# Optimization experiments

Measured on AMD Instinct MI355X. Metric: run time of the kernel, lower is better.

The kernel has to match this reference:

```python
import jax, jax.numpy as jnp
import numpy as np
import math


def _sinusoidal_pe(seq_len, hidden_dim, dtype):
    pos = jnp.arange(seq_len, dtype=jnp.float32)[:, None]              # [S,1]
    div = jnp.exp(jnp.arange(0, hidden_dim, 2, dtype=jnp.float32) * (-math.log(10000.0) / hidden_dim))  # [H/2]
    ang = pos * div                                                    # [S,H/2]
    pe = jnp.stack([jnp.sin(ang), jnp.cos(ang)], axis=-1).reshape(seq_len, hidden_dim)  # interleave sin/cos
    return pe.astype(dtype)


def setup_inputs() -> dict:
    key = jax.random.key(0)
    ks = jax.random.split(key, 12)
    B, S, H = 4, 2048, 1024
    scale = 1.0 / math.sqrt(H)
    inp = {
        "x": jax.random.normal(ks[0], (B, S, H), dtype=jnp.float32),
        "mask": jax.random.randint(ks[1], (B, S, S), 0, 2, dtype=jnp.int32),
        "Wq": jax.random.normal(ks[2], (H, H), dtype=jnp.float32) * scale,
        "bq": jax.random.normal(ks[3], (H,), dtype=jnp.float32) * 0.02,
        "Wk": jax.random.normal(ks[4], (H, H), dtype=jnp.float32) * scale,
        "bk": jax.random.normal(ks[5], (H,), dtype=jnp.float32) * 0.02,
        "Wv": jax.random.normal(ks[6], (H, H), dtype=jnp.float32) * scale,
        "bv": jax.random.normal(ks[7], (H,), dtype=jnp.float32) * 0.02,
        "pos_bias": jax.random.normal(ks[8], (S, S), dtype=jnp.float32),
        "Wo": jax.random.normal(ks[9], (H, H), dtype=jnp.float32) * scale,
        "bo": jax.random.normal(ks[10], (H,), dtype=jnp.float32) * 0.02,
        "gamma": jnp.ones((H,), dtype=jnp.float32),
        "beta": jnp.zeros((H,), dtype=jnp.float32),
    }
    return inp


def reference(x, mask, Wq, bq, Wk, bk, Wv, bv, pos_bias, Wo, bo, gamma, beta):
    B, S, H = x.shape
    scale = math.sqrt(H)
    pe = _sinusoidal_pe(S, H, x.dtype)                  # [S,H]
    xp = x + pe[None, :, :]                             # [B,S,H]
    # torch Linear: y = x @ W.T + b
    q = jnp.einsum('bsh,oh->bso', xp, Wq) + bq
    k = jnp.einsum('bsh,oh->bso', xp, Wk) + bk
    v = jnp.einsum('bsh,oh->bso', xp, Wv) + bv
    scores = jnp.einsum('bqh,bkh->bqk', q, k) / scale   # [B,S,S]
    scores = scores + pos_bias[None, :S, :S]
    scores = jnp.where(mask == 0, jnp.asarray(-1e9, scores.dtype), scores)
    attn = jax.nn.softmax(scores, axis=-1)              # dropout = identity (eval mode)
    context = jnp.einsum('bqk,bkh->bqh', attn, v)
    out = jnp.einsum('bsh,oh->bso', context, Wo) + bo
    # LayerNorm(out + x)
    h = out + x
    mu = jnp.mean(h, axis=-1, keepdims=True)
    var = jnp.var(h, axis=-1, keepdims=True)
    normed = (h - mu) * jax.lax.rsqrt(var + 1e-5) * gamma + beta
    return normed, attn
```

## Files before the change

### kernel.cpp

```cpp
#include <hip/hip_runtime.h>
#include <hip/hip_bf16.h>
#include <math.h>

typedef __hip_bfloat16 bf16;
typedef __bf16 bf16x8 __attribute__((ext_vector_type(8)));
typedef float f32x4 __attribute__((ext_vector_type(4)));

static constexpr int  B_  = 4, S_ = 2048, H_ = 1024;
static constexpr long BSH = (long)B_ * S_ * H_;
static constexpr long SH  = (long)S_ * H_;
static constexpr long SS  = (long)S_ * S_;
static constexpr long HH  = (long)H_ * H_;

#define GLOAD_LDS16(gp, lp)                                                          \
  __builtin_amdgcn_global_load_lds((__attribute__((address_space(1))) void*)(gp),    \
                                   (__attribute__((address_space(3))) void*)(lp),    \
                                   16, 0, 0)

#define BARRIER() do { __builtin_amdgcn_s_barrier(); asm volatile("" ::: "memory"); } while (0)

template <int N> __device__ __forceinline__ void waitcnt_vm() {
  if constexpr (N == 0)      asm volatile("s_waitcnt vmcnt(0)" ::: "memory");
  else if constexpr (N == 3) asm volatile("s_waitcnt vmcnt(3)" ::: "memory");
  else if constexpr (N == 4) asm volatile("s_waitcnt vmcnt(4)" ::: "memory");
  else if constexpr (N == 6) asm volatile("s_waitcnt vmcnt(6)" ::: "memory");
  else if constexpr (N == 8) asm volatile("s_waitcnt vmcnt(8)" ::: "memory");
}

__device__ __forceinline__ float wave_reduce_sum(float v) {
#pragma unroll
  for (int o = 32; o; o >>= 1) v += __shfl_xor(v, o, 64);
  return v;
}
__device__ __forceinline__ float bf16r(float v) {
  return __bfloat162float(__float2bfloat16(v));
}

__global__ void prep_kernel(const float* __restrict__ Wq, const float* __restrict__ Wk,
                            const float* __restrict__ Wv, const float* __restrict__ Wo,
                            bf16* __restrict__ wdst,
                            const float* __restrict__ x, bf16* __restrict__ xpb) {
  const int bx  = blockIdx.x;
  const int tid = threadIdx.x;
  if (bx < 4096) {
    const int w = bx >> 10;
    const float* src = (w == 0) ? Wq : (w == 1) ? Wk : (w == 2) ? Wv : Wo;
    bf16* d = wdst + (long)w * HH;
    const int idx = ((bx & 1023) << 8) + tid;
    const float4 f = ((const float4*)src)[idx];
    d[idx * 4 + 0] = __float2bfloat16(f.x);
    d[idx * 4 + 1] = __float2bfloat16(f.y);
    d[idx * 4 + 2] = __float2bfloat16(f.z);
    d[idx * 4 + 3] = __float2bfloat16(f.w);
  } else {
    const long idx = (((long)(bx - 4096)) << 8) + tid;
    const int  i   = (int)(idx & (H_ / 2 - 1));
    const long bs  = idx >> 9;
    const int  s   = (int)(bs & (S_ - 1));
    const float div = __expf((float)(2 * i) * (-9.210340371976184f / (float)H_));
    const float ang = (float)s * div;
    const float2 xv = ((const float2*)x)[idx];
    xpb[idx * 2 + 0] = __float2bfloat16(xv.x + sinf(ang));
    xpb[idx * 2 + 1] = __float2bfloat16(xv.y + cosf(ang));
  }
}

template <int MODE, int BN>
__global__ __launch_bounds__(512, 2)
void gemm_nt(const bf16* __restrict__ A, long strideA,
             const bf16* __restrict__ Bm, long strideB,
             bf16* __restrict__ Cb, float* __restrict__ Cf, long sC,
             int M, int N, int K,
             const float* __restrict__ bias0,
             const float* __restrict__ bias1,
             const float* __restrict__ bias2,
             const float* __restrict__ pos_bias,
             const int* __restrict__ mask,
             const float* __restrict__ xres,
             const float* __restrict__ inv_sum) {
  constexpr int BM = 256, BK = 32;
  constexpr int FN    = BN / 64;
  constexpr int LPT_B = BN * BK * 2 / 8192;
  constexpr int LPT   = 2 + LPT_B;

  __shared__ bf16 sA[4][BM * BK];
  __shared__ bf16 sB[4][BN * BK];

  const int t    = threadIdx.x;
  const int lane = t & 63;
  const int wave = t >> 6;
  const int wm   = wave >> 2;
  const int wn   = wave & 3;
  const int z    = blockIdx.z;
  const int m0   = blockIdx.x * BM;
  const int n0   = blockIdx.y * BN;

  const bf16* Ab = A  + (long)z * strideA;
  const bf16* Bb = Bm + (long)z * strideB;

  const int rS  = t >> 2, pS = t & 3;
  const int swS = (rS >> 1) & 3;
  const bf16* gA0 = Ab + (long)(m0 + rS)       * K + (pS ^ swS) * 8;
  const bf16* gA1 = Ab + (long)(m0 + rS + 128) * K + (pS ^ swS) * 8;
  const bf16* gB0 = Bb + (long)(n0 + rS)       * K + (pS ^ swS) * 8;
  const bf16* gB1 = Bb + (long)(n0 + rS + 128) * K + (pS ^ swS) * 8;

  auto stage = [&](int tileIdx) {
    const int buf = tileIdx & 3;
    const int k0  = tileIdx * BK;
    GLOAD_LDS16(gA0 + k0, &sA[buf][t * 8]);
    GLOAD_LDS16(gA1 + k0, &sA[buf][(t + 512) * 8]);
    GLOAD_LDS16(gB0 + k0, &sB[buf][t * 8]);
    if constexpr (BN == 256) GLOAD_LDS16(gB1 + k0, &sB[buf][(t + 512) * 8]);
  };

  const int fr  = lane & 15;
  const int cqs = ((lane >> 4) << 4) ^ (((fr >> 1) & 3) << 4);

  f32x4 acc[8][FN] = {};

  auto tile_compute = [&](int buf) {
    const char* bA = (const char*)&sA[buf][0];
    const char* bB = (const char*)&sB[buf][0];
    bf16x8 bfv[FN];
#pragma unroll
    for (int j = 0; j < FN; ++j)
      bfv[j] = *(const bf16x8*)(bB + (wn * (BN / 4) + j * 16 + fr) * 64 + cqs);
#pragma unroll
    for (int qm = 0; qm < 2; ++qm) {
      bf16x8 af[4];
#pragma unroll
      for (int i = 0; i < 4; ++i)
        af[i] = *(const bf16x8*)(bA + (wm * 128 + qm * 64 + i * 16 + fr) * 64 + cqs);
      __builtin_amdgcn_s_setprio(1);
#pragma unroll
      for (int i = 0; i < 4; ++i)
#pragma unroll
        for (int j = 0; j < FN; ++j)
          acc[qm * 4 + i][j] =
              __builtin_amdgcn_mfma_f32_16x16x32_bf16(af[i], bfv[j], acc[qm * 4 + i][j], 0, 0, 0);
      __builtin_amdgcn_s_setprio(0);
    }
  };

  const int nkt = K / BK;
  stage(0); stage(1); stage(2);
  for (int kt = 0; kt < nkt - 2; ++kt) {
    waitcnt_vm<2 * LPT>();
    BARRIER();
    if (kt + 3 < nkt) stage(kt + 3);
    tile_compute(kt & 3);
  }
  waitcnt_vm<LPT>();
  BARRIER();
  tile_compute((nkt - 2) & 3);
  waitcnt_vm<0>();
  BARRIER();
  tile_compute((nkt - 1) & 3);

  const float* biasz = (MODE == 0) ? ((z == 0) ? bias0 : (z == 1) ? bias1 : bias2) : bias0;

  const int cc = lane & 15;
  const int cr = (lane >> 4) * 4;
#pragma unroll
  for (int mi = 0; mi < 8; ++mi) {
    const int rowb = m0 + wm * 128 + mi * 16 + cr;
#pragma unroll
    for (int j = 0; j < FN; ++j) {
      const int col = n0 + wn * (BN / 4) + j * 16 + cc;
#pragma unroll
      for (int r = 0; r < 4; ++r) {
        const int  row  = rowb + r;
        const long loff = (long)row * N + col;
        const long off  = (long)z * sC + loff;
        const float v   = acc[mi][j][r];
        if (MODE == 0) {
          Cb[off] = __float2bfloat16(v + biasz[col]);
        } else if (MODE == 1) {
          float sc = v * (1.0f / 32.0f) + pos_bias[loff];
          if (mask[off] == 0) sc = -1e9f;
          Cb[off] = __float2bfloat16(__expf(fminf(sc, 60.0f)));
        } else if (MODE == 2) {
          Cb[off] = __float2bfloat16(v * inv_sum[z * S_ + row]);
        } else {
          Cf[off] = v + biasz[col] + xres[off];
        }
      }
    }
  }
}

__global__ void transpose_kernel(const bf16* __restrict__ v, bf16* __restrict__ vT) {
  __shared__ bf16 tile[64][65];
  const int b     = blockIdx.z;
  const int sBase = blockIdx.x * 64;
  const int hBase = blockIdx.y * 64;
  const bf16* vb  = v  + (long)b * SH;
  bf16*       vTb = vT + (long)b * SH;
  const int tx = threadIdx.x & 63;
  const int ty = threadIdx.x >> 6;
#pragma unroll
  for (int r = ty; r < 64; r += 4)
    tile[r][tx] = vb[(long)(sBase + r) * H_ + hBase + tx];
  __syncthreads();
#pragma unroll
  for (int r = ty; r < 64; r += 4)
    vTb[(long)(hBase + r) * S_ + sBase + tx] = tile[tx][r];
}

__global__ void rownorm_kernel(const bf16* __restrict__ E, float* __restrict__ attn_f,
                               float* __restrict__ inv_sum) {
  const long row = blockIdx.x;
  const int  tid = threadIdx.x;
  const uint4 d = *(const uint4*)(E + row * (long)S_ + tid * 8);
  float ev[8];
  ev[0] = __uint_as_float(d.x << 16); ev[1] = __uint_as_float(d.x & 0xffff0000u);
  ev[2] = __uint_as_float(d.y << 16); ev[3] = __uint_as_float(d.y & 0xffff0000u);
  ev[4] = __uint_as_float(d.z << 16); ev[5] = __uint_as_float(d.z & 0xffff0000u);
  ev[6] = __uint_as_float(d.w << 16); ev[7] = __uint_as_float(d.w & 0xffff0000u);
  float s = 0.f;
#pragma unroll
  for (int i = 0; i < 8; ++i) s += ev[i];
  s = wave_reduce_sum(s);
  __shared__ float red[4];
  if ((tid & 63) == 0) red[tid >> 6] = s;
  __syncthreads();
  const float inv = 1.0f / fmaxf(red[0] + red[1] + red[2] + red[3], 1e-30f);
  if (tid == 0) inv_sum[row] = inv;
  float4 o0, o1;
  o0.x = bf16r(ev[0] * inv); o0.y = bf16r(ev[1] * inv);
  o0.z = bf16r(ev[2] * inv); o0.w = bf16r(ev[3] * inv);
  o1.x = bf16r(ev[4] * inv); o1.y = bf16r(ev[5] * inv);
  o1.z = bf16r(ev[6] * inv); o1.w = bf16r(ev[7] * inv);
  float4* dst = (float4*)(attn_f + row * (long)S_ + tid * 8);
  dst[0] = o0;
  dst[1] = o1;
}

__global__ void ln_kernel(float* __restrict__ h, const float* __restrict__ gamma,
                          const float* __restrict__ beta) {
  const long row = blockIdx.x;
  float* hr = h + row * (long)H_;
  const int tid = threadIdx.x;
  float v[4];
  float s = 0.f;
#pragma unroll
  for (int i = 0; i < 4; ++i) { v[i] = hr[tid + i * 256]; s += v[i]; }
  s = wave_reduce_sum(s);
  __shared__ float redA[4], redB[4];
  if ((tid & 63) == 0) redA[tid >> 6] = s;
  __syncthreads();
  const float mu = (redA[0] + redA[1] + redA[2] + redA[3]) * (1.0f / H_);
  float vs = 0.f;
#pragma unroll
  for (int i = 0; i < 4; ++i) { const float d = v[i] - mu; vs += d * d; }
  vs = wave_reduce_sum(vs);
  if ((tid & 63) == 0) redB[tid >> 6] = vs;
  __syncthreads();
  const float var  = (redB[0] + redB[1] + redB[2] + redB[3]) * (1.0f / H_);
  const float rstd = rsqrtf(var + 1e-5f);
#pragma unroll
  for (int i = 0; i < 4; ++i) {
    const int c = tid + i * 256;
    hr[c] = bf16r((v[i] - mu) * rstd * gamma[c] + beta[c]);
  }
}

extern "C" void kernel_launch(void* const* d_in, const int* in_sizes, int n_in,
                              void* d_out, int out_size, void* d_ws, size_t ws_size,
                              hipStream_t stream) {
  const float* x        = (const float*)d_in[0];
  const int*   mask     = (const int*)d_in[1];
  const float* Wq       = (const float*)d_in[2];
  const float* bq       = (const float*)d_in[3];
  const float* Wk       = (const float*)d_in[4];
  const float* bk       = (const float*)d_in[5];
  const float* Wv       = (const float*)d_in[6];
  const float* bv       = (const float*)d_in[7];
  const float* pos_bias = (const float*)d_in[8];
  const float* Wo       = (const float*)d_in[9];
  const float* bo       = (const float*)d_in[10];
  const float* gamma    = (const float*)d_in[11];
  const float* beta     = (const float*)d_in[12];

  float* normed_f = (float*)d_out;
  float* attn_f   = (float*)((char*)d_out + ((size_t)32 << 20));

  const size_t MiB = (size_t)1 << 20;
  bf16*  xpb     = (bf16*)d_ws;
  bf16*  q_b     = (bf16*)((char*)d_ws +  16 * MiB);
  bf16*  kbuf    = (bf16*)((char*)d_ws +  32 * MiB);
  bf16*  vbuf    = (bf16*)((char*)d_ws +  48 * MiB);
  bf16*  vT      = (bf16*)((char*)d_ws +  64 * MiB);
  bf16*  ctx     = (bf16*)((char*)d_ws +  80 * MiB);
  bf16*  attn_b  = (bf16*)((char*)d_ws +  96 * MiB);
  bf16*  wts     = (bf16*)((char*)d_ws + 128 * MiB);
  float* inv_sum = (float*)((char*)d_ws + 136 * MiB);
  bf16* Wqb = wts, *Wob = wts + 3 * HH;

  const int MQKV = B_ * S_;

  prep_kernel<<<dim3(20480), 256, 0, stream>>>(Wq, Wk, Wv, Wo, wts, x, xpb);

  gemm_nt<0, 128><<<dim3(32, 8, 3), 512, 0, stream>>>(xpb, 0, Wqb, HH, q_b, nullptr, BSH,
                                                      MQKV, H_, H_, bq, bk, bv,
                                                      nullptr, nullptr, nullptr, nullptr);

  transpose_kernel<<<dim3(S_ / 64, H_ / 64, B_), 256, 0, stream>>>(vbuf, vT);

  gemm_nt<1, 256><<<dim3(8, 8, 4), 512, 0, stream>>>(q_b, SH, kbuf, SH,
                                                     attn_b, nullptr, SS,
                                                     S_, S_, H_, nullptr, nullptr, nullptr,
                                                     pos_bias, mask, nullptr, nullptr);

  rownorm_kernel<<<B_ * S_, 256, 0, stream>>>(attn_b, attn_f, inv_sum);

  gemm_nt<2, 128><<<dim3(8, 8, 4), 512, 0, stream>>>(attn_b, SS, vT, SH,
                                                     ctx, nullptr, SH,
                                                     S_, H_, S_, nullptr, nullptr, nullptr,
                                                     nullptr, nullptr, nullptr, inv_sum);

  gemm_nt<3, 128><<<dim3(32, 8, 1), 512, 0, stream>>>(ctx, 0, Wob, 0, nullptr, normed_f, 0,
                                                      MQKV, H_, H_, bo, nullptr, nullptr,
                                                      nullptr, nullptr, x, nullptr);

  ln_kernel<<<B_ * S_, 256, 0, stream>>>(normed_f, gamma, beta);
}
```

Before: 482.3 us.

## Transpose GEMM tile shape to BN=256 and split stage loads across two compute halves

The GEMM template now fixes BN=256 and makes BM the parameter, so the 128-wide GEMMs become 128x256 tiles and their grids are reshaped to match. The main loop is flattened and each k-step is split into two MFMA halves with a barrier between them. A-tile prefetch is issued before the first half and B-tile prefetch before the second, to spread global-to-LDS traffic across compute. The extra barrier per iteration adds sync cost, and the changed tile aspect shifts the balance of A and B reuse.

```diff
diff --git a/kernel.cpp b/kernel.cpp
--- a/kernel.cpp
+++ b/kernel.cpp
@@ -65,7 +65,7 @@
   }
 }
 
-template <int MODE, int BN>
+template <int MODE, int BM>
 __global__ __launch_bounds__(512, 2)
 void gemm_nt(const bf16* __restrict__ A, long strideA,
              const bf16* __restrict__ Bm, long strideB,
@@ -78,13 +78,14 @@
              const int* __restrict__ mask,
              const float* __restrict__ xres,
              const float* __restrict__ inv_sum) {
-  constexpr int BM = 256, BK = 32;
-  constexpr int FN    = BN / 64;
-  constexpr int LPT_B = BN * BK * 2 / 8192;
-  constexpr int LPT   = 2 + LPT_B;
-
-  __shared__ bf16 sA[4][BM * BK];
-  __shared__ bf16 sB[4][BN * BK];
+  constexpr int BN = 256, BK = 32;
+  constexpr int MR    = BM / 32;
+  constexpr int MR2   = MR / 2;
+  constexpr int LPT_A = BM / 128;
+  constexpr int LPT   = LPT_A + 2;
+
+  __shared__ bf16 sAb[4][BM * BK];
+  __shared__ bf16 sBb[4][BN * BK];
 
   const int t    = threadIdx.x;
   const int lane = t & 63;
@@ -105,69 +106,77 @@
   const bf16* gB0 = Bb + (long)(n0 + rS)       * K + (pS ^ swS) * 8;
   const bf16* gB1 = Bb + (long)(n0 + rS + 128) * K + (pS ^ swS) * 8;
 
-  auto stage = [&](int tileIdx) {
-    const int buf = tileIdx & 3;
-    const int k0  = tileIdx * BK;
-    GLOAD_LDS16(gA0 + k0, &sA[buf][t * 8]);
-    GLOAD_LDS16(gA1 + k0, &sA[buf][(t + 512) * 8]);
-    GLOAD_LDS16(gB0 + k0, &sB[buf][t * 8]);
-    if constexpr (BN == 256) GLOAD_LDS16(gB1 + k0, &sB[buf][(t + 512) * 8]);
+  auto stageA = [&](int tile) {
+    const int buf = tile & 3, k0 = tile * BK;
+    GLOAD_LDS16(gA0 + k0, &sAb[buf][t * 8]);
+    if constexpr (BM == 256) GLOAD_LDS16(gA1 + k0, &sAb[buf][(t + 512) * 8]);
+  };
+  auto stageB = [&](int tile) {
+    const int buf = tile & 3, k0 = tile * BK;
+    GLOAD_LDS16(gB0 + k0, &sBb[buf][t * 8]);
+    GLOAD_LDS16(gB1 + k0, &sBb[buf][(t + 512) * 8]);
   };
 
   const int fr  = lane & 15;
   const int cqs = ((lane >> 4) << 4) ^ (((fr >> 1) & 3) << 4);
 
-  f32x4 acc[8][FN] = {};
-
-  auto tile_compute = [&](int buf) {
-    const char* bA = (const char*)&sA[buf][0];
-    const char* bB = (const char*)&sB[buf][0];
-    bf16x8 bfv[FN];
-#pragma unroll
-    for (int j = 0; j < FN; ++j)
-      bfv[j] = *(const bf16x8*)(bB + (wn * (BN / 4) + j * 16 + fr) * 64 + cqs);
-#pragma unroll
-    for (int qm = 0; qm < 2; ++qm) {
-      bf16x8 af[4];
-#pragma unroll
-      for (int i = 0; i < 4; ++i)
-        af[i] = *(const bf16x8*)(bA + (wm * 128 + qm * 64 + i * 16 + fr) * 64 + cqs);
-      __builtin_amdgcn_s_setprio(1);
-#pragma unroll
-      for (int i = 0; i < 4; ++i)
-#pragma unroll
-        for (int j = 0; j < FN; ++j)
-          acc[qm * 4 + i][j] =
-              __builtin_amdgcn_mfma_f32_16x16x32_bf16(af[i], bfv[j], acc[qm * 4 + i][j], 0, 0, 0);
-      __builtin_amdgcn_s_setprio(0);
-    }
-  };
+  f32x4 acc[MR][4] = {};
 
   const int nkt = K / BK;
-  stage(0); stage(1); stage(2);
-  for (int kt = 0; kt < nkt - 2; ++kt) {
-    waitcnt_vm<2 * LPT>();
+  stageA(0); stageB(0);
+  stageA(1); stageB(1);
+  stageA(2); stageB(2);
+
+  for (int kt = 0; kt < nkt; ++kt) {
+    if (kt < nkt - 2)      waitcnt_vm<2 * LPT>();
+    else if (kt == nkt - 2) waitcnt_vm<LPT>();
+    else                    waitcnt_vm<0>();
     BARRIER();
-    if (kt + 3 < nkt) stage(kt + 3);
-    tile_compute(kt & 3);
+    const bool st = (kt + 3 < nkt);
+    if (st) stageA(kt + 3);
+
+    const char* bA = (const char*)&sAb[kt & 3][0];
+    const char* bB = (const char*)&sBb[kt & 3][0];
+    bf16x8 bfv[4], af[MR2];
+#pragma unroll
+    for (int j = 0; j < 4; ++j)
+      bfv[j] = *(const bf16x8*)(bB + (wn * 64 + j * 16 + fr) * 64 + cqs);
+#pragma unroll
+    for (int i = 0; i < MR2; ++i)
+      af[i] = *(const bf16x8*)(bA + (wm * (BM / 2) + i * 16 + fr) * 64 + cqs);
+    __builtin_amdgcn_s_setprio(1);
+#pragma unroll
+    for (int i = 0; i < MR2; ++i)
+#pragma unroll
+      for (int j = 0; j < 4; ++j)
+        acc[i][j] = __builtin_amdgcn_mfma_f32_16x16x32_bf16(af[i], bfv[j], acc[i][j], 0, 0, 0);
+    __builtin_amdgcn_s_setprio(0);
+
+    BARRIER();
+    if (st) stageB(kt + 3);
+#pragma unroll
+    for (int i = 0; i < MR2; ++i)
+      af[i] = *(const bf16x8*)(bA + (wm * (BM / 2) + (MR2 + i) * 16 + fr) * 64 + cqs);
+    __builtin_amdgcn_s_setprio(1);
+#pragma unroll
+    for (int i = 0; i < MR2; ++i)
+#pragma unroll
+      for (int j = 0; j < 4; ++j)
+        acc[MR2 + i][j] =
+            __builtin_amdgcn_mfma_f32_16x16x32_bf16(af[i], bfv[j], acc[MR2 + i][j], 0, 0, 0);
+    __builtin_amdgcn_s_setprio(0);
   }
-  waitcnt_vm<LPT>();
-  BARRIER();
-  tile_compute((nkt - 2) & 3);
-  waitcnt_vm<0>();
-  BARRIER();
-  tile_compute((nkt - 1) & 3);
 
   const float* biasz = (MODE == 0) ? ((z == 0) ? bias0 : (z == 1) ? bias1 : bias2) : bias0;
 
   const int cc = lane & 15;
   const int cr = (lane >> 4) * 4;
 #pragma unroll
-  for (int mi = 0; mi < 8; ++mi) {
-    const int rowb = m0 + wm * 128 + mi * 16 + cr;
-#pragma unroll
-    for (int j = 0; j < FN; ++j) {
-      const int col = n0 + wn * (BN / 4) + j * 16 + cc;
+  for (int mi = 0; mi < MR; ++mi) {
+    const int rowb = m0 + wm * (BM / 2) + mi * 16 + cr;
+#pragma unroll
+    for (int j = 0; j < 4; ++j) {
+      const int col = n0 + wn * 64 + j * 16 + cc;
 #pragma unroll
       for (int r = 0; r < 4; ++r) {
         const int  row  = rowb + r;
@@ -302,7 +311,7 @@
 
   prep_kernel<<<dim3(20480), 256, 0, stream>>>(Wq, Wk, Wv, Wo, wts, x, xpb);
 
-  gemm_nt<0, 128><<<dim3(32, 8, 3), 512, 0, stream>>>(xpb, 0, Wqb, HH, q_b, nullptr, BSH,
+  gemm_nt<0, 128><<<dim3(64, 4, 3), 512, 0, stream>>>(xpb, 0, Wqb, HH, q_b, nullptr, BSH,
                                                       MQKV, H_, H_, bq, bk, bv,
                                                       nullptr, nullptr, nullptr, nullptr);
 
@@ -315,12 +324,12 @@
 
   rownorm_kernel<<<B_ * S_, 256, 0, stream>>>(attn_b, attn_f, inv_sum);
 
-  gemm_nt<2, 128><<<dim3(8, 8, 4), 512, 0, stream>>>(attn_b, SS, vT, SH,
-                                                     ctx, nullptr, SH,
-                                                     S_, H_, S_, nullptr, nullptr, nullptr,
-                                                     nullptr, nullptr, nullptr, inv_sum);
-
-  gemm_nt<3, 128><<<dim3(32, 8, 1), 512, 0, stream>>>(ctx, 0, Wob, 0, nullptr, normed_f, 0,
+  gemm_nt<2, 128><<<dim3(16, 4, 4), 512, 0, stream>>>(attn_b, SS, vT, SH,
+                                                      ctx, nullptr, SH,
+                                                      S_, H_, S_, nullptr, nullptr, nullptr,
+                                                      nullptr, nullptr, nullptr, inv_sum);
+
+  gemm_nt<3, 128><<<dim3(64, 4, 1), 512, 0, stream>>>(ctx, 0, Wob, 0, nullptr, normed_f, 0,
                                                       MQKV, H_, H_, bo, nullptr, nullptr,
                                                       nullptr, nullptr, x, nullptr);
 
```

Result: slower. 495.6 us (+2.7%).
